# Performance work log

Hardware: AMD Instinct MI355X
Metric: run time of the kernel (lower is better)

## Reference

```python
import jax, jax.numpy as jnp
import numpy as np
from jax import lax

IMG = 256   # model img_size
O = 7       # adaptive pool output size (out_size)
R = 32      # number of ROIs
B = 8       # batch
CF = 32     # UNet output channels
FOUT = 512  # fc out_features


def _conv(x, w, b):
    y = lax.conv_general_dilated(x, w, (1, 1), 'SAME',
                                 dimension_numbers=('NCHW', 'OIHW', 'NCHW'))
    return y + b[None, :, None, None]


def _pool(x):
    return lax.reduce_window(x, -jnp.inf, lax.max, (1, 1, 2, 2), (1, 1, 2, 2), 'VALID')


def _up(x):
    return jnp.repeat(jnp.repeat(x, 2, axis=2), 2, axis=3)


def _unet(x, p):
    r = jax.nn.relu
    e1 = r(_conv(r(_conv(x, p['e1w1'], p['e1b1'])), p['e1w2'], p['e1b2']))          # [B,32,H,W]
    e2 = r(_conv(r(_conv(_pool(e1), p['e2w1'], p['e2b1'])), p['e2w2'], p['e2b2']))  # [B,64,H/2,W/2]
    bo = r(_conv(r(_conv(_pool(e2), p['bw1'], p['bb1'])), p['bw2'], p['bb2']))      # [B,128,H/4,W/4]
    u2 = r(_conv(_up(bo), p['u2w'], p['u2b']))                                      # [B,64,H/2,W/2]
    d2 = r(_conv(r(_conv(jnp.concatenate([u2, e2], 1), p['d2w1'], p['d2b1'])), p['d2w2'], p['d2b2']))
    u1 = r(_conv(_up(d2), p['u1w'], p['u1b']))                                      # [B,32,H,W]
    d1 = r(_conv(r(_conv(jnp.concatenate([u1, e1], 1), p['d1w1'], p['d1b1'])), p['d1w2'], p['d1b2']))
    return _conv(d1, p['fw'], p['fb'])                                              # [B,CF,H,W]


def _adaptive_pool(ii, boxes):
    # Exact F.adaptive_avg_pool2d bins via an integral image.
    # ii: [B,C,H+1,W+1] (zero-padded 2D cumsum); boxes: [R,4] int (x1,y1,x2,y2).
    i = jnp.arange(O)
    h = boxes[:, 3] - boxes[:, 1]
    w = boxes[:, 2] - boxes[:, 0]
    sy = boxes[:, 1:2] + (i[None, :] * h[:, None]) // O            # floor(i*h/O)
    ey = boxes[:, 1:2] + ((i[None, :] + 1) * h[:, None] + O - 1) // O  # ceil((i+1)*h/O)
    sx = boxes[:, 0:1] + (i[None, :] * w[:, None]) // O
    ex = boxes[:, 0:1] + ((i[None, :] + 1) * w[:, None] + O - 1) // O
    yA, yB = sy[:, :, None], ey[:, :, None]   # [R,O,1]
    xA, xB = sx[:, None, :], ex[:, None, :]   # [R,1,O]
    s = ii[:, :, yB, xB] - ii[:, :, yA, xB] - ii[:, :, yB, xA] + ii[:, :, yA, xA]  # [B,C,R,O,O]
    area = ((ey - sy)[:, :, None] * (ex - sx)[:, None, :]).astype(ii.dtype)        # [R,O,O]
    return s / area[None, None]


def _forward(x, rois, p):
    H, W = x.shape[2], x.shape[3]
    xs, ys = IMG // H, IMG // W  # matches torch: x_scale, y_scale = img_size//m, img_size//n
    boxes = rois // jnp.array([xs, ys, xs, ys], dtype=rois.dtype)
    f = _unet(x, p)                                   # [B,CF,H,W]
    ii = jnp.pad(jnp.cumsum(jnp.cumsum(f, axis=2), axis=3),
                 ((0, 0), (0, 0), (1, 0), (1, 0)))    # integral image [B,CF,H+1,W+1]
    rp = _adaptive_pool(ii, boxes)                    # [B,CF,R,O,O]
    roi_feat = jnp.transpose(rp, (0, 2, 1, 3, 4)).reshape(x.shape[0], boxes.shape[0] * f.shape[1], O, O)
    gbox = jnp.array([[0, 0, W, H]], dtype=boxes.dtype)
    gpool = _adaptive_pool(ii, gbox)[:, :, 0]         # [B,CF,O,O]
    out = jnp.concatenate([gpool, roi_feat], axis=1)  # [B,(R+1)*CF,O,O]
    out = out.reshape(out.shape[0], out.shape[1], O * O)
    return jnp.einsum('bnk,fk->bnf', out, p['fcw']) + p['fcb']


_PNAMES = ['e1w1','e1b1','e1w2','e1b2','e2w1','e2b1','e2w2','e2b2','bw1','bb1','bw2','bb2',
           'u2w','u2b','d2w1','d2b1','d2w2','d2b2','u1w','u1b','d1w1','d1b1','d1w2','d1b2',
           'fw','fb','fcw','fcb']


def setup_inputs() -> dict:
    key = jax.random.key(0)
    ks = jax.random.split(key, 32)

    def w(k, shape):
        fan = int(np.prod(shape[1:]))
        return jax.random.normal(k, shape, jnp.float32) * np.sqrt(2.0 / fan)

    d = {}
    d['x'] = jax.random.normal(ks[0], (B, 3, IMG, IMG), jnp.float32)
    xy1 = jax.random.randint(ks[1], (R, 2), 0, 192)
    wh = jax.random.randint(ks[2], (R, 2), 16, 64)
    d['rois'] = jnp.concatenate([xy1, xy1 + wh], axis=1).astype(jnp.int32)  # (x1,y1,x2,y2)

    shapes = {'e1w1': (32, 3, 3, 3), 'e1w2': (32, 32, 3, 3),
              'e2w1': (64, 32, 3, 3), 'e2w2': (64, 64, 3, 3),
              'bw1': (128, 64, 3, 3), 'bw2': (128, 128, 3, 3),
              'u2w': (64, 128, 3, 3),
              'd2w1': (64, 128, 3, 3), 'd2w2': (64, 64, 3, 3),
              'u1w': (32, 64, 3, 3),
              'd1w1': (32, 64, 3, 3), 'd1w2': (32, 32, 3, 3),
              'fw': (CF, 32, 1, 1),
              'fcw': (FOUT, O * O)}
    i = 3
    for n, s in shapes.items():
        d[n] = w(ks[i], s); i += 1
        bn = n.replace('w', 'b', 1) if 'w' in n else n
        d[bn] = jnp.zeros((s[0],), jnp.float32)
    d['fcb'] = jnp.zeros((FOUT,), jnp.float32)
    return d


def reference(x, rois, e1w1, e1b1, e1w2, e1b2, e2w1, e2b1, e2w2, e2b2,
              bw1, bb1, bw2, bb2, u2w, u2b, d2w1, d2b1, d2w2, d2b2,
              u1w, u1b, d1w1, d1b1, d1w2, d1b2, fw, fb, fcw, fcb):
    p = dict(e1w1=e1w1, e1b1=e1b1, e1w2=e1w2, e1b2=e1b2, e2w1=e2w1, e2b1=e2b1,
             e2w2=e2w2, e2b2=e2b2, bw1=bw1, bb1=bb1, bw2=bw2, bb2=bb2,
             u2w=u2w, u2b=u2b, d2w1=d2w1, d2b1=d2b1, d2w2=d2w2, d2b2=d2b2,
             u1w=u1w, u1b=u1b, d1w1=d1w1, d1b1=d1b1, d1w2=d1w2, d1b2=d1b2,
             fw=fw, fb=fb, fcw=fcw, fcb=fcb)
    return _forward(x, rois, p)
```

## Files before the change

kernel.cpp:

```cpp
#include <hip/hip_runtime.h>

typedef _Float16 half8 __attribute__((ext_vector_type(8)));
typedef float f32x4 __attribute__((ext_vector_type(4)));
typedef float f32x16 __attribute__((ext_vector_type(16)));

__device__ __forceinline__ unsigned short f2h(float f) {
    _Float16 h = (_Float16)f;
    return __builtin_bit_cast(unsigned short, h);
}
__device__ __forceinline__ float h2f(unsigned short u) {
    return (float)__builtin_bit_cast(_Float16, u);
}

__device__ __forceinline__ void lds_load16(const uint4* g, uint4* l) {
    __builtin_amdgcn_global_load_lds(
        (const __attribute__((address_space(1))) unsigned int*)g,
        (__attribute__((address_space(3))) unsigned int*)l, 16, 0, 0);
}

struct PrepArgs {
    const float* src[13];
    unsigned dstOff[13];
    int Cout[13], Cin[13];
    unsigned off[14];
};

__global__ void prep_all_k(PrepArgs a, char* __restrict__ WT)
{
    unsigned t = blockIdx.x * 256 + threadIdx.x;
    if (t >= a.off[13]) return;
    int l = 0;
    while (t >= a.off[l + 1]) ++l;
    unsigned e = t - a.off[l];
    if (l < 11) {
        int j = e & 7; unsigned r = e >> 3;
        const int Cout = a.Cout[l], Cin = a.Cin[l];
        int co = r % Cout; r /= Cout;
        int oct = r & 3; r >>= 2;
        int pos = r % 9; int ck = r / 9;
        int ci = ck * 32 + oct * 8 + j;
        ((unsigned short*)(WT + a.dstOff[l]))[e] =
            f2h(a.src[l][((size_t)co * Cin + ci) * 9 + pos]);
    } else if (l == 11) {
        int k = e >> 9, ff = e & 511;
        ((float*)(WT + a.dstOff[l]))[e] = a.src[l][ff * 49 + k];
    } else {
        int j = e & 7, co = (e >> 3) & 31, koct = e >> 8;
        ((unsigned short*)(WT + a.dstOff[l]))[e] =
            f2h(a.src[l][co * 32 + koct * 8 + j]);
    }
}

template<int BM, int TW, int TH, int LW, int UP>
__global__ __launch_bounds__(256, 2) void convm4_k(
    const uint4* __restrict__ in1, int C1g,
    const uint4* __restrict__ in2, int C2g,
    const uint4* __restrict__ wt,
    const float* __restrict__ bias,
    unsigned short* __restrict__ out,
    int Cout, int relu, const uint4* __restrict__ zp)
{
    constexpr int NM = BM / 16;
    constexpr int NN = (TW * TH) / 64;
    constexpr int CG = TW / 16;
    constexpr int RQ = NN / CG;
    static_assert(RQ == 2, "row-reuse layout needs 2 rows/wave");
    constexpr int Wf = 1 << LW, Hf = Wf;
    constexpr int WC = TW + 2, HR = TH + 2;
    constexpr int IN_GR = 4 * HR * WC;
    constexpr int LTW = (TW == 64) ? 6 : 5;
    constexpr int sH = UP ? (Hf >> 1) : Hf;
    constexpr int sW = UP ? (Wf >> 1) : Wf;
    __shared__ uint4 smem[IN_GR + 36 * BM];

    const int tid = threadIdx.x;
    const int lane = tid & 63, wv = tid >> 6;
    const int ng = Cout / BM;
    const int b = blockIdx.z / ng, cg = blockIdx.z % ng;
    const int x0 = blockIdx.x * TW, y0 = blockIdx.y * TH;
    const int NCK = (C1g + C2g) / 4;

    f32x4 acc[NM][NN];
#pragma unroll
    for (int m = 0; m < NM; ++m)
#pragma unroll
        for (int n = 0; n < NN; ++n) acc[m][n] = (f32x4){0.f, 0.f, 0.f, 0.f};

    const int l15 = lane & 15, l4 = lane >> 4;
    const int laneB = l4 * HR * WC + l15;
    const int laneA = l4 * BM + l15;

    for (int ck = 0; ck < NCK; ++ck) {
        if (ck) __syncthreads();
        {
            const uint4* src; int cg0, srcCg;
            if (ck * 4 < C1g) { src = in1; cg0 = ck * 4; srcCg = C1g; }
            else              { src = in2; cg0 = ck * 4 - C1g; srcCg = C2g; }
            for (int i = tid; i < IN_GR; i += 256) {
                int oct = i / (HR * WC);
                int rem = i - oct * (HR * WC);
                int row = rem / WC;
                int col = rem - row * WC;
                int gy = y0 + row - 1, gx = x0 + col - 1;
                int sy = UP ? (gy >> 1) : gy, sx = UP ? (gx >> 1) : gx;
                const uint4* ga = ((unsigned)gy < (unsigned)Hf && (unsigned)gx < (unsigned)Wf)
                    ? src + ((((size_t)b * sH + sy) * sW + sx) * srcCg + cg0 + oct)
                    : zp + (i & 63);
                lds_load16(ga, &smem[i]);
            }
        }
        {
            const uint4* wck = wt + (size_t)ck * 36 * Cout + (size_t)cg * BM;
            for (int i = tid; i < 36 * BM; i += 256) {
                int seg = i / BM, col = i - seg * BM;
                lds_load16(wck + seg * Cout + col, &smem[IN_GR + i]);
            }
        }
        __syncthreads();
        const half8* sB = (const half8*)smem;
        const half8* sA = (const half8*)(smem + IN_GR);
#pragma unroll
        for (int dc = 0; dc < 3; ++dc) {
            half8 br[RQ + 2][CG];
#pragma unroll
            for (int r = 0; r < RQ + 2; ++r)
#pragma unroll
                for (int c2 = 0; c2 < CG; ++c2)
                    br[r][c2] = sB[(wv * RQ + r) * WC + c2 * 16 + dc + laneB];
#pragma unroll
            for (int dr = 0; dr < 3; ++dr) {
                half8 af[NM];
#pragma unroll
                for (int m = 0; m < NM; ++m)
                    af[m] = sA[(dr * 3 + dc) * 4 * BM + m * 16 + laneA];
#pragma unroll
                for (int m = 0; m < NM; ++m)
#pragma unroll
                    for (int rq = 0; rq < RQ; ++rq)
#pragma unroll
                        for (int c2 = 0; c2 < CG; ++c2)
                            acc[m][rq * CG + c2] = __builtin_amdgcn_mfma_f32_16x16x32_f16(
                                af[m], br[rq + dr][c2], acc[m][rq * CG + c2], 0, 0, 0);
            }
        }
    }

#pragma unroll
    for (int m = 0; m < NM; ++m) {
        const int co0 = cg * BM + m * 16 + l4 * 4;
        const float4 bs = *(const float4*)(bias + co0);
#pragma unroll
        for (int n = 0; n < NN; ++n) {
            const int pix = wv * (NN * 16) + n * 16 + l15;
            const int y = y0 + (pix >> LTW), x = x0 + (pix & (TW - 1));
            float v0 = acc[m][n][0] + bs.x;
            float v1 = acc[m][n][1] + bs.y;
            float v2 = acc[m][n][2] + bs.z;
            float v3 = acc[m][n][3] + bs.w;
            if (relu) {
                v0 = fmaxf(v0, 0.f); v1 = fmaxf(v1, 0.f);
                v2 = fmaxf(v2, 0.f); v3 = fmaxf(v3, 0.f);
            }
            uint2 pk;
            pk.x = (unsigned)f2h(v0) | ((unsigned)f2h(v1) << 16);
            pk.y = (unsigned)f2h(v2) | ((unsigned)f2h(v3) << 16);
            *(uint2*)(out + (((size_t)b * Hf + y) * Wf + x) * Cout + co0) = pk;
        }
    }
}

__global__ __launch_bounds__(256) void conv0_k(
    const float* __restrict__ in, const float* __restrict__ w,
    const float* __restrict__ bias, unsigned short* __restrict__ out)
{
    __shared__ float s_in[3][18][18];
    const int tx = threadIdx.x, ty = threadIdx.y;
    const int tid = ty * 16 + tx;
    const int b = blockIdx.z >> 2;
    const int coBase = (blockIdx.z & 3) * 8;
    const int bx = blockIdx.x * 16, by = blockIdx.y * 16;

    for (int i = tid; i < 3 * 18 * 18; i += 256) {
        int cc = i / 324, r = i % 324;
        int ly = r / 18, lx = r % 18;
        int gy = by + ly - 1, gx = bx + lx - 1;
        float v = 0.f;
        if ((unsigned)gy < 256u && (unsigned)gx < 256u)
            v = in[(((size_t)(b * 3 + cc)) << 16) + (gy << 8) + gx];
        ((float*)s_in)[i] = v;
    }
    __syncthreads();
    float acc[8];
#pragma unroll
    for (int k = 0; k < 8; ++k) acc[k] = 0.f;
    for (int cc = 0; cc < 3; ++cc) {
        float v[9];
#pragma unroll
        for (int dh = 0; dh < 3; ++dh)
#pragma unroll
            for (int dw = 0; dw < 3; ++dw)
                v[dh * 3 + dw] = s_in[cc][ty + dh][tx + dw];
        const float* wp = w + ((size_t)coBase * 3 + cc) * 9;
#pragma unroll
        for (int k = 0; k < 8; ++k) {
            const float* wk = wp + (size_t)k * 27;
            float a = acc[k];
#pragma unroll
            for (int j = 0; j < 9; ++j) a = fmaf(v[j], wk[j], a);
            acc[k] = a;
        }
    }
    const int h = by + ty, ww = bx + tx;
    unsigned short* op = out + (((size_t)(b * 256 + h)) * 256 + ww) * 32 + coBase;
#pragma unroll
    for (int k = 0; k < 8; ++k)
        op[k] = f2h(fmaxf(acc[k] + bias[coBase + k], 0.f));
}

__global__ void poolh_k(const uint4* __restrict__ in, uint4* __restrict__ out,
                        int Ho, int Wo, int C8, int total)
{
    int i = blockIdx.x * 256 + threadIdx.x;
    if (i >= total) return;
    int oct = i % C8; int p = i / C8;
    int x = p % Wo; p /= Wo;
    int y = p % Ho; int b = p / Ho;
    const int H = Ho * 2, W = Wo * 2;
    size_t g = (((size_t)b * H + 2 * y) * W + 2 * x) * C8 + oct;
    uint4 v00 = in[g], v01 = in[g + C8];
    uint4 v10 = in[g + (size_t)W * C8], v11 = in[g + (size_t)W * C8 + C8];
    const unsigned short* a0 = (const unsigned short*)&v00;
    const unsigned short* a1 = (const unsigned short*)&v01;
    const unsigned short* a2 = (const unsigned short*)&v10;
    const unsigned short* a3 = (const unsigned short*)&v11;
    uint4 res; unsigned short* rp = (unsigned short*)&res;
#pragma unroll
    for (int j = 0; j < 8; ++j)
        rp[j] = f2h(fmaxf(fmaxf(h2f(a0[j]), h2f(a1[j])), fmaxf(h2f(a2[j]), h2f(a3[j]))));
    out[(((size_t)b * Ho + y) * Wo + x) * C8 + oct] = res;
}

__global__ __launch_bounds__(256) void conv1x1f_k(
    const uint4* __restrict__ in, const uint4* __restrict__ w16,
    const float* __restrict__ bias, unsigned short* __restrict__ f)
{
    __shared__ uint4 sIn[1024];
    __shared__ uint4 sW[128];
    __shared__ float sb[32];
    const int tid = threadIdx.x;
    const int lane = tid & 63, wv = tid >> 6;
    const int l31 = lane & 31, l5 = lane >> 5;
    const int y = blockIdx.x, b = blockIdx.y;

    const uint4* ip = in + (((size_t)b * 256 + y) * 256) * 4;
#pragma unroll
    for (int it = 0; it < 4; ++it)
        lds_load16(ip + tid + it * 256, &sIn[tid + it * 256]);
    if (tid < 128) lds_load16(w16 + tid, &sW[tid]);
    if (tid < 32) sb[tid] = bias[tid];
    __syncthreads();

    const half8* hW = (const half8*)sW;
    const half8* hIn = (const half8*)sIn;
    half8 af0 = hW[l5 * 32 + l31];
    half8 af1 = hW[(2 + l5) * 32 + l31];
    unsigned short* fp_ = f + ((size_t)b * 32) * 65536 + (size_t)y * 256;
#pragma unroll
    for (int g = 0; g < 2; ++g) {
        const int p0 = wv * 64 + g * 32;
        half8 bf0 = hIn[(p0 + l31) * 4 + l5];
        half8 bf1 = hIn[(p0 + l31) * 4 + 2 + l5];
        f32x16 acc;
#pragma unroll
        for (int q = 0; q < 16; ++q) acc[q] = 0.f;
        acc = __builtin_amdgcn_mfma_f32_32x32x16_f16(af0, bf0, acc, 0, 0, 0);
        acc = __builtin_amdgcn_mfma_f32_32x32x16_f16(af1, bf1, acc, 0, 0, 0);
#pragma unroll
        for (int r = 0; r < 16; ++r) {
            const int co = (r & 3) + 8 * (r >> 2) + 4 * l5;
            fp_[(size_t)co * 65536 + p0 + l31] = f2h(acc[r] + sb[co]);
        }
    }
}

__global__ __launch_bounds__(256) void gcol_k(
    const unsigned short* __restrict__ f, float* __restrict__ colsumG)
{
    const int ki = blockIdx.x;
    const int c  = blockIdx.y;
    const int b  = blockIdx.z;
    const int x  = threadIdx.x;
    const int sy = (ki * 256) / 7, ey = ((ki + 1) * 256 + 6) / 7;
    const unsigned short* pl = f + (size_t)(b * 32 + c) * 65536;
    float s = 0.f;
    for (int y = sy; y < ey; ++y)
        s += h2f(pl[(size_t)y * 256 + x]);
    colsumG[((size_t)(b * 32 + c) * 7 + ki) * 256 + x] = s;
}

__global__ __launch_bounds__(64) void gpool2_k(
    const float* __restrict__ colsumG, float* __restrict__ pooled)
{
    const int c = blockIdx.x, b = blockIdx.y;
    const int lane = threadIdx.x;
    if (lane >= 49) return;
    const int ki = lane / 7, kj = lane % 7;
    const int sy = (ki * 256) / 7, ey = ((ki + 1) * 256 + 6) / 7;
    const int sx = (kj * 256) / 7, ex = ((kj + 1) * 256 + 6) / 7;
    const float* cs = colsumG + ((size_t)(b * 32 + c) * 7 + ki) * 256;
    float s = 0.f;
    for (int x = sx; x < ex; ++x) s += cs[x];
    pooled[((size_t)b * 1056 + c) * 49 + lane] = s / (float)((ey - sy) * (ex - sx));
}

__global__ __launch_bounds__(64) void roi_k(
    const unsigned short* __restrict__ f, const int* __restrict__ rois,
    float* __restrict__ pooled)
{
    __shared__ float colsum[7][64];
    const int n = 32 + blockIdx.x, b = blockIdx.y;
    const int lane = threadIdx.x;
    const int r = (n - 32) >> 5;
    const int c = (n - 32) & 31;
    const int x1 = rois[r * 4 + 0], y1 = rois[r * 4 + 1];
    const int x2 = rois[r * 4 + 2], y2 = rois[r * 4 + 3];
    const int h = y2 - y1, w = x2 - x1;
    const unsigned short* pl = f + (size_t)(b * 32 + c) * 65536;
    if (lane < w) {
        const int x = x1 + lane;
#pragma unroll
        for (int ki = 0; ki < 7; ++ki) {
            const int sy = y1 + (ki * h) / 7, ey = y1 + ((ki + 1) * h + 6) / 7;
            float s = 0.f;
            for (int y = sy; y < ey; ++y)
                s += h2f(pl[(size_t)y * 256 + x]);
            colsum[ki][lane] = s;
        }
    }
    __syncthreads();
    if (lane >= 49) return;
    const int ki = lane / 7, kj = lane % 7;
    const int sy = y1 + (ki * h) / 7, ey = y1 + ((ki + 1) * h + 6) / 7;
    const int sxo = (kj * w) / 7, exo = ((kj + 1) * w + 6) / 7;
    float s = 0.f;
    for (int j = sxo; j < exo; ++j) s += colsum[ki][j];
    pooled[((size_t)b * 1056 + n) * 49 + lane] = s / (float)((ey - sy) * (exo - sxo));
}

__global__ __launch_bounds__(512) void fc_k(
    const float* __restrict__ pooled, const float* __restrict__ fcwT,
    const float* __restrict__ fcb, float* __restrict__ out)
{
    const int nt = blockIdx.x, b = blockIdx.y;
    const int f = threadIdx.x;
    float wr[49];
#pragma unroll
    for (int k = 0; k < 49; ++k) wr[k] = fcwT[k * 512 + f];
    const float base = fcb[f];
    const float* pr = pooled + ((size_t)b * 1056 + nt * 16) * 49;
    float* op = out + (((size_t)b * 1056 + nt * 16)) * 512 + f;
#pragma unroll
    for (int j = 0; j < 16; ++j) {
        float a = base;
#pragma unroll
        for (int k = 0; k < 49; ++k)
            a = fmaf(pr[j * 49 + k], wr[k], a);
        op[(size_t)j * 512] = a;
    }
}

extern "C" void kernel_launch(void* const* d_in, const int* in_sizes, int n_in,
                              void* d_out, int out_size, void* d_ws, size_t ws_size,
                              hipStream_t stream)
{
    const float* x    = (const float*)d_in[0];
    const int*   rois = (const int*)d_in[1];
    const float* e1w1 = (const float*)d_in[2];
    const float* e1b1 = (const float*)d_in[3];
    const float* e1w2 = (const float*)d_in[4];
    const float* e1b2 = (const float*)d_in[5];
    const float* e2w1 = (const float*)d_in[6];
    const float* e2b1 = (const float*)d_in[7];
    const float* e2w2 = (const float*)d_in[8];
    const float* e2b2 = (const float*)d_in[9];
    const float* bw1  = (const float*)d_in[10];
    const float* bb1  = (const float*)d_in[11];
    const float* bw2  = (const float*)d_in[12];
    const float* bb2  = (const float*)d_in[13];
    const float* u2w  = (const float*)d_in[14];
    const float* u2b  = (const float*)d_in[15];
    const float* d2w1 = (const float*)d_in[16];
    const float* d2b1 = (const float*)d_in[17];
    const float* d2w2 = (const float*)d_in[18];
    const float* d2b2 = (const float*)d_in[19];
    const float* u1w  = (const float*)d_in[20];
    const float* u1b  = (const float*)d_in[21];
    const float* d1w1 = (const float*)d_in[22];
    const float* d1b1 = (const float*)d_in[23];
    const float* d1w2 = (const float*)d_in[24];
    const float* d1b2 = (const float*)d_in[25];
    const float* fw   = (const float*)d_in[26];
    const float* fb   = (const float*)d_in[27];
    const float* fcw  = (const float*)d_in[28];
    const float* fcb  = (const float*)d_in[29];

    char* wsb = (char*)d_ws;
    char* WT = wsb;
    char* A  = wsb + 4194304;
    char* D  = A + 33554432;
    char* E  = D + 16777216;
    char* Bb = E + 16777216;
    char* C  = Bb + 33554432;
    char* F  = C + 8388608;
    float* fcwT   = (float*)(WT + 1179648);
    unsigned short* fw16 = (unsigned short*)(WT + 2097152);
    uint4* zp     = (uint4*)(WT + 4194304 - 8192);
    unsigned short* fpl = (unsigned short*)F;
    float* pooled = (float*)C;
    float* colsumG = (float*)(C + 2097152);
    hipMemsetAsync(zp, 0, 8192, stream);

    const float* wsrc[11] = {e1w2, e2w1, e2w2, bw1, bw2, u2w, d2w1, d2w2, u1w, d1w1, d1w2};
    const int wco[11] = {32, 64, 64, 128, 128, 64, 64, 64, 32, 32, 32};
    const int wci[11] = {32, 32, 64, 64, 128, 128, 128, 64, 64, 64, 32};
    size_t woff[11]; size_t o = 0;
    PrepArgs pa;
    unsigned eoff = 0;
    for (int i = 0; i < 11; ++i) {
        woff[i] = o; o += (size_t)wco[i] * wci[i] * 18;
        pa.src[i] = wsrc[i]; pa.dstOff[i] = (unsigned)woff[i];
        pa.Cout[i] = wco[i]; pa.Cin[i] = wci[i];
        pa.off[i] = eoff; eoff += (unsigned)(wco[i] * wci[i] * 9);
    }
    pa.src[11] = fcw; pa.dstOff[11] = 1179648; pa.Cout[11] = 0; pa.Cin[11] = 0;
    pa.off[11] = eoff; eoff += 49 * 512;
    pa.src[12] = fw; pa.dstOff[12] = 2097152; pa.Cout[12] = 0; pa.Cin[12] = 0;
    pa.off[12] = eoff; eoff += 4096;
    pa.off[13] = eoff;
    hipLaunchKernelGGL(prep_all_k, dim3((eoff + 255) / 256), dim3(256), 0, stream, pa, WT);
    auto WP = [&](int i) { return (const uint4*)(WT + woff[i]); };

    #define CV1(i1,C1,i2,C2,wi,bs,ot,Cout,up,rl) \
        hipLaunchKernelGGL((convm4_k<32,32,8,8,up>), dim3(8,32,8*((Cout)/32)), dim3(256), 0, stream, \
            (const uint4*)(i1), (C1)/8, (const uint4*)(i2), (C2)/8, WP(wi), bs, \
            (unsigned short*)(ot), Cout, rl, zp)
    #define CV2(i1,C1,i2,C2,wi,bs,ot,Cout,up,rl) \
        hipLaunchKernelGGL((convm4_k<32,32,8,7,up>), dim3(4,16,8*((Cout)/32)), dim3(256), 0, stream, \
            (const uint4*)(i1), (C1)/8, (const uint4*)(i2), (C2)/8, WP(wi), bs, \
            (unsigned short*)(ot), Cout, rl, zp)
    #define CV3(i1,C1,i2,C2,wi,bs,ot,Cout,up,rl) \
        hipLaunchKernelGGL((convm4_k<32,32,8,6,up>), dim3(2,8,8*((Cout)/32)), dim3(256), 0, stream, \
            (const uint4*)(i1), (C1)/8, (const uint4*)(i2), (C2)/8, WP(wi), bs, \
            (unsigned short*)(ot), Cout, rl, zp)

    hipLaunchKernelGGL(conv0_k, dim3(16, 16, 32), dim3(16, 16), 0, stream,
                       x, e1w1, e1b1, (unsigned short*)A);
    CV1(A, 32, nullptr, 0, 0, e1b2, Bb, 32, 0, 1);
    {
        int N = 8 * 128 * 128 * 4;
        hipLaunchKernelGGL(poolh_k, dim3((N + 255) / 256), dim3(256), 0, stream,
                           (const uint4*)Bb, (uint4*)C, 128, 128, 4, N);
    }
    CV2(C, 32, nullptr, 0, 1, e2b1, A, 64, 0, 1);
    CV2(A, 64, nullptr, 0, 2, e2b2, D, 64, 0, 1);
    {
        int N = 8 * 64 * 64 * 8;
        hipLaunchKernelGGL(poolh_k, dim3((N + 255) / 256), dim3(256), 0, stream,
                           (const uint4*)D, (uint4*)C, 64, 64, 8, N);
    }
    CV3(C, 64, nullptr, 0, 3, bb1, E, 128, 0, 1);
    CV3(E, 128, nullptr, 0, 4, bb2, A, 128, 0, 1);
    CV2(A, 128, nullptr, 0, 5, u2b, E, 64, 1, 1);
    CV2(E, 64, D, 64, 6, d2b1, A, 64, 0, 1);
    CV2(A, 64, nullptr, 0, 7, d2b2, D, 64, 0, 1);
    CV1(D, 64, nullptr, 0, 8, u1b, A, 32, 1, 1);
    CV1(A, 32, Bb, 32, 9, d1b1, D, 32, 0, 1);
    CV1(D, 32, nullptr, 0, 10, d1b2, Bb, 32, 0, 1);
    hipLaunchKernelGGL(conv1x1f_k, dim3(256, 8), dim3(256), 0, stream,
                       (const uint4*)Bb, (const uint4*)fw16, fb, fpl);
    hipLaunchKernelGGL(gcol_k, dim3(7, 32, 8), dim3(256), 0, stream, fpl, colsumG);
    hipLaunchKernelGGL(roi_k, dim3(1024, 8), dim3(64), 0, stream, fpl, rois, pooled);
    hipLaunchKernelGGL(gpool2_k, dim3(32, 8), dim3(64), 0, stream, colsumG, pooled);
    hipLaunchKernelGGL(fc_k, dim3(66, 8), dim3(512), 0, stream,
                       pooled, fcwT, fcb, (float*)d_out);
    #undef CV1
    #undef CV2
    #undef CV3
}
```

Before: 366.2 us.

## Fuse 2x2 max-pool into conv epilogue and widen CV2 channel block to 64

Adds a POOL template flag to the MFMA conv kernel, so the epilogue also computes the 2x2 max over its two output rows and adjacent lanes and writes the pooled tensor directly. This removes the two standalone pooling kernels and their re-read of the full-resolution activations. Separately, the CV2 layers now use a 64-channel output block per workgroup instead of 32, which halves their grid in z and increases register and LDS use per block. Pooling in fp32 before rounding to half could differ by rounding from the old pool-on-half path, though the results should match in practice.

New measurement: 354.0 us, median of 3. -3.3%, faster.

```diff
diff --git a/kernel.cpp b/kernel.cpp
--- a/kernel.cpp
+++ b/kernel.cpp
@@ -51,14 +51,15 @@
     }
 }
 
-template<int BM, int TW, int TH, int LW, int UP>
+template<int BM, int TW, int TH, int LW, int UP, int POOL>
 __global__ __launch_bounds__(256, 2) void convm4_k(
     const uint4* __restrict__ in1, int C1g,
     const uint4* __restrict__ in2, int C2g,
     const uint4* __restrict__ wt,
     const float* __restrict__ bias,
     unsigned short* __restrict__ out,
-    int Cout, int relu, const uint4* __restrict__ zp)
+    int Cout, int relu, const uint4* __restrict__ zp,
+    unsigned short* __restrict__ pout)
 {
     constexpr int NM = BM / 16;
     constexpr int NN = (TW * TH) / 64;
@@ -150,21 +151,47 @@
         const int co0 = cg * BM + m * 16 + l4 * 4;
         const float4 bs = *(const float4*)(bias + co0);
 #pragma unroll
-        for (int n = 0; n < NN; ++n) {
-            const int pix = wv * (NN * 16) + n * 16 + l15;
-            const int y = y0 + (pix >> LTW), x = x0 + (pix & (TW - 1));
-            float v0 = acc[m][n][0] + bs.x;
-            float v1 = acc[m][n][1] + bs.y;
-            float v2 = acc[m][n][2] + bs.z;
-            float v3 = acc[m][n][3] + bs.w;
-            if (relu) {
-                v0 = fmaxf(v0, 0.f); v1 = fmaxf(v1, 0.f);
-                v2 = fmaxf(v2, 0.f); v3 = fmaxf(v3, 0.f);
+        for (int c2 = 0; c2 < CG; ++c2) {
+            float pv0, pv1, pv2, pv3;
+#pragma unroll
+            for (int rq = 0; rq < RQ; ++rq) {
+                const int n = rq * CG + c2;
+                const int pix = wv * (NN * 16) + n * 16 + l15;
+                const int y = y0 + (pix >> LTW), x = x0 + (pix & (TW - 1));
+                float v0 = acc[m][n][0] + bs.x;
+                float v1 = acc[m][n][1] + bs.y;
+                float v2 = acc[m][n][2] + bs.z;
+                float v3 = acc[m][n][3] + bs.w;
+                if (relu) {
+                    v0 = fmaxf(v0, 0.f); v1 = fmaxf(v1, 0.f);
+                    v2 = fmaxf(v2, 0.f); v3 = fmaxf(v3, 0.f);
+                }
+                uint2 pk;
+                pk.x = (unsigned)f2h(v0) | ((unsigned)f2h(v1) << 16);
+                pk.y = (unsigned)f2h(v2) | ((unsigned)f2h(v3) << 16);
+                *(uint2*)(out + (((size_t)b * Hf + y) * Wf + x) * Cout + co0) = pk;
+                if (POOL) {
+                    if (rq == 0) { pv0 = v0; pv1 = v1; pv2 = v2; pv3 = v3; }
+                    else {
+                        pv0 = fmaxf(pv0, v0); pv1 = fmaxf(pv1, v1);
+                        pv2 = fmaxf(pv2, v2); pv3 = fmaxf(pv3, v3);
+                    }
+                }
             }
-            uint2 pk;
-            pk.x = (unsigned)f2h(v0) | ((unsigned)f2h(v1) << 16);
-            pk.y = (unsigned)f2h(v2) | ((unsigned)f2h(v3) << 16);
-            *(uint2*)(out + (((size_t)b * Hf + y) * Wf + x) * Cout + co0) = pk;
+            if (POOL) {
+                float q0 = fmaxf(pv0, __shfl_xor(pv0, 1));
+                float q1 = fmaxf(pv1, __shfl_xor(pv1, 1));
+                float q2 = fmaxf(pv2, __shfl_xor(pv2, 1));
+                float q3 = fmaxf(pv3, __shfl_xor(pv3, 1));
+                if ((l15 & 1) == 0) {
+                    const int xp = (x0 >> 1) + ((c2 * 16 + l15) >> 1);
+                    const int yp = (y0 >> 1) + wv;
+                    uint2 pk;
+                    pk.x = (unsigned)f2h(q0) | ((unsigned)f2h(q1) << 16);
+                    pk.y = (unsigned)f2h(q2) | ((unsigned)f2h(q3) << 16);
+                    *(uint2*)(pout + (((size_t)b * (Hf >> 1) + yp) * (Wf >> 1) + xp) * Cout + co0) = pk;
+                }
+            }
         }
     }
 }
@@ -215,29 +242,6 @@
 #pragma unroll
     for (int k = 0; k < 8; ++k)
         op[k] = f2h(fmaxf(acc[k] + bias[coBase + k], 0.f));
-}
-
-__global__ void poolh_k(const uint4* __restrict__ in, uint4* __restrict__ out,
-                        int Ho, int Wo, int C8, int total)
-{
-    int i = blockIdx.x * 256 + threadIdx.x;
-    if (i >= total) return;
-    int oct = i % C8; int p = i / C8;
-    int x = p % Wo; p /= Wo;
-    int y = p % Ho; int b = p / Ho;
-    const int H = Ho * 2, W = Wo * 2;
-    size_t g = (((size_t)b * H + 2 * y) * W + 2 * x) * C8 + oct;
-    uint4 v00 = in[g], v01 = in[g + C8];
-    uint4 v10 = in[g + (size_t)W * C8], v11 = in[g + (size_t)W * C8 + C8];
-    const unsigned short* a0 = (const unsigned short*)&v00;
-    const unsigned short* a1 = (const unsigned short*)&v01;
-    const unsigned short* a2 = (const unsigned short*)&v10;
-    const unsigned short* a3 = (const unsigned short*)&v11;
-    uint4 res; unsigned short* rp = (unsigned short*)&res;
-#pragma unroll
-    for (int j = 0; j < 8; ++j)
-        rp[j] = f2h(fmaxf(fmaxf(h2f(a0[j]), h2f(a1[j])), fmaxf(h2f(a2[j]), h2f(a3[j]))));
-    out[(((size_t)b * Ho + y) * Wo + x) * C8 + oct] = res;
 }
 
 __global__ __launch_bounds__(256) void conv1x1f_k(
@@ -440,42 +444,32 @@
     hipLaunchKernelGGL(prep_all_k, dim3((eoff + 255) / 256), dim3(256), 0, stream, pa, WT);
     auto WP = [&](int i) { return (const uint4*)(WT + woff[i]); };
 
-    #define CV1(i1,C1,i2,C2,wi,bs,ot,Cout,up,rl) \
-        hipLaunchKernelGGL((convm4_k<32,32,8,8,up>), dim3(8,32,8*((Cout)/32)), dim3(256), 0, stream, \
+    #define CV1(i1,C1,i2,C2,wi,bs,ot,Cout,up,rl,pl,po) \
+        hipLaunchKernelGGL((convm4_k<32,32,8,8,up,pl>), dim3(8,32,8*((Cout)/32)), dim3(256), 0, stream, \
             (const uint4*)(i1), (C1)/8, (const uint4*)(i2), (C2)/8, WP(wi), bs, \
-            (unsigned short*)(ot), Cout, rl, zp)
-    #define CV2(i1,C1,i2,C2,wi,bs,ot,Cout,up,rl) \
-        hipLaunchKernelGGL((convm4_k<32,32,8,7,up>), dim3(4,16,8*((Cout)/32)), dim3(256), 0, stream, \
+            (unsigned short*)(ot), Cout, rl, zp, (unsigned short*)(po))
+    #define CV2(i1,C1,i2,C2,wi,bs,ot,Cout,up,rl,pl,po) \
+        hipLaunchKernelGGL((convm4_k<64,32,8,7,up,pl>), dim3(4,16,8*((Cout)/64)), dim3(256), 0, stream, \
             (const uint4*)(i1), (C1)/8, (const uint4*)(i2), (C2)/8, WP(wi), bs, \
-            (unsigned short*)(ot), Cout, rl, zp)
+            (unsigned short*)(ot), Cout, rl, zp, (unsigned short*)(po))
     #define CV3(i1,C1,i2,C2,wi,bs,ot,Cout,up,rl) \
-        hipLaunchKernelGGL((convm4_k<32,32,8,6,up>), dim3(2,8,8*((Cout)/32)), dim3(256), 0, stream, \
+        hipLaunchKernelGGL((convm4_k<32,32,8,6,up,0>), dim3(2,8,8*((Cout)/32)), dim3(256), 0, stream, \
             (const uint4*)(i1), (C1)/8, (const uint4*)(i2), (C2)/8, WP(wi), bs, \
-            (unsigned short*)(ot), Cout, rl, zp)
+            (unsigned short*)(ot), Cout, rl, zp, (unsigned short*)nullptr)
 
     hipLaunchKernelGGL(conv0_k, dim3(16, 16, 32), dim3(16, 16), 0, stream,
                        x, e1w1, e1b1, (unsigned short*)A);
-    CV1(A, 32, nullptr, 0, 0, e1b2, Bb, 32, 0, 1);
-    {
-        int N = 8 * 128 * 128 * 4;
-        hipLaunchKernelGGL(poolh_k, dim3((N + 255) / 256), dim3(256), 0, stream,
-                           (const uint4*)Bb, (uint4*)C, 128, 128, 4, N);
-    }
-    CV2(C, 32, nullptr, 0, 1, e2b1, A, 64, 0, 1);
-    CV2(A, 64, nullptr, 0, 2, e2b2, D, 64, 0, 1);
-    {
-        int N = 8 * 64 * 64 * 8;
-        hipLaunchKernelGGL(poolh_k, dim3((N + 255) / 256), dim3(256), 0, stream,
-                           (const uint4*)D, (uint4*)C, 64, 64, 8, N);
-    }
+    CV1(A, 32, nullptr, 0, 0, e1b2, Bb, 32, 0, 1, 1, C);
+    CV2(C, 32, nullptr, 0, 1, e2b1, A, 64, 0, 1, 0, nullptr);
+    CV2(A, 64, nullptr, 0, 2, e2b2, D, 64, 0, 1, 1, C);
     CV3(C, 64, nullptr, 0, 3, bb1, E, 128, 0, 1);
     CV3(E, 128, nullptr, 0, 4, bb2, A, 128, 0, 1);
-    CV2(A, 128, nullptr, 0, 5, u2b, E, 64, 1, 1);
-    CV2(E, 64, D, 64, 6, d2b1, A, 64, 0, 1);
-    CV2(A, 64, nullptr, 0, 7, d2b2, D, 64, 0, 1);
-    CV1(D, 64, nullptr, 0, 8, u1b, A, 32, 1, 1);
-    CV1(A, 32, Bb, 32, 9, d1b1, D, 32, 0, 1);
-    CV1(D, 32, nullptr, 0, 10, d1b2, Bb, 32, 0, 1);
+    CV2(A, 128, nullptr, 0, 5, u2b, E, 64, 1, 1, 0, nullptr);
+    CV2(E, 64, D, 64, 6, d2b1, A, 64, 0, 1, 0, nullptr);
+    CV2(A, 64, nullptr, 0, 7, d2b2, D, 64, 0, 1, 0, nullptr);
+    CV1(D, 64, nullptr, 0, 8, u1b, A, 32, 1, 1, 0, nullptr);
+    CV1(A, 32, Bb, 32, 9, d1b1, D, 32, 0, 1, 0, nullptr);
+    CV1(D, 32, nullptr, 0, 10, d1b2, Bb, 32, 0, 1, 0, nullptr);
     hipLaunchKernelGGL(conv1x1f_k, dim3(256, 8), dim3(256), 0, stream,
                        (const uint4*)Bb, (const uint4*)fw16, fb, fpl);
     hipLaunchKernelGGL(gcol_k, dim3(7, 32, 8), dim3(256), 0, stream, fpl, colsumG);
```
